# Kernel optimization log

Measured on AMD Instinct MI355X. Metric: run time of the kernel, lower is better.

Reference implementation:

```python
import jax, jax.numpy as jnp
import numpy as np

N_NODES = 50000
N_EDGES = 3200000
N_GRAPHS = 50
IN_FEATS, HIDDEN, OUT_FEATS = 5, 64, 2


def setup_inputs() -> dict:
    key = jax.random.key(0)
    ks = jax.random.split(key, 10)
    x = jax.random.normal(ks[0], (N_NODES, IN_FEATS), dtype=jnp.float32)
    edge_index = jax.random.randint(ks[1], (2, N_EDGES), 0, N_NODES, dtype=jnp.int64)
    edge_attr = jax.random.uniform(ks[2], (N_EDGES, 1), dtype=jnp.float32)
    batch = jnp.sort(jax.random.randint(ks[3], (N_NODES,), 0, N_GRAPHS, dtype=jnp.int64))
    s1 = 1.0 / np.sqrt(IN_FEATS)
    s2 = 1.0 / np.sqrt(HIDDEN)
    W1 = jax.random.uniform(ks[4], (IN_FEATS, HIDDEN), jnp.float32, -s1, s1)
    b1 = jnp.zeros((HIDDEN,), jnp.float32)
    W2 = jax.random.uniform(ks[5], (HIDDEN, HIDDEN), jnp.float32, -s2, s2)
    b2 = jnp.zeros((HIDDEN,), jnp.float32)
    Wo = jax.random.uniform(ks[6], (HIDDEN, OUT_FEATS), jnp.float32, -s2, s2)
    bo = jax.random.uniform(ks[7], (OUT_FEATS,), jnp.float32, -s2, s2)
    return {"x": x, "edge_index": edge_index, "edge_attr": edge_attr, "batch": batch,
            "W1": W1, "b1": b1, "W2": W2, "b2": b2, "Wo": Wo, "bo": bo}


def _gcn_conv(x, src, dst, ew, W, b):
    # symmetric normalization: D^{-1/2} (A + I) D^{-1/2}, weighted degrees
    deg = jax.ops.segment_sum(ew, dst, num_segments=N_NODES)
    dinv = jnp.where(deg > 0, jax.lax.rsqrt(jnp.where(deg > 0, deg, 1.0)), 0.0)
    norm = dinv[src] * ew * dinv[dst]  # [E+N]
    h = x @ W                           # transform before propagate (PyG order)
    msg = h[src] * norm[:, None]        # gather + scale per edge
    out = jax.ops.segment_sum(msg, dst, num_segments=N_NODES)
    return out + b


def reference(x, edge_index, edge_attr, batch, W1, b1, W2, b2, Wo, bo):
    ew = edge_attr.squeeze(-1)
    loop = jnp.arange(N_NODES, dtype=edge_index.dtype)  # add self-loops (GCNConv default)
    src = jnp.concatenate([edge_index[0], loop])
    dst = jnp.concatenate([edge_index[1], loop])
    ew = jnp.concatenate([ew, jnp.ones((N_NODES,), ew.dtype)])
    h = jax.nn.relu(_gcn_conv(x, src, dst, ew, W1, b1))
    h = jax.nn.relu(_gcn_conv(h, src, dst, ew, W2, b2))
    # global mean pool over graphs
    sums = jax.ops.segment_sum(h, batch, num_segments=N_GRAPHS)
    cnt = jax.ops.segment_sum(jnp.ones((N_NODES,), h.dtype), batch, num_segments=N_GRAPHS)
    pooled = sums / jnp.maximum(cnt, 1.0)[:, None]
    return pooled @ Wo + bo  # [N_GRAPHS, OUT_FEATS]
```

## Files before the change

kernel.cpp:

```cpp
#include <hip/hip_runtime.h>
#include <hip/hip_fp16.h>

#define N_NODES 50000
#define N_EDGES 3200000
#define N_GRAPHS 50
#define IN_F 5
#define HID 64
#define OUT_F 2

#define BKT_SHIFT 5
#define BKT_W 32
#define NBKT 1563
#define NB1 250
#define EPB 12800
#define CAP 2560
#define TILE_SHIFT 12
#define NTILE 16
#define NBIN (BKT_W * NTILE)
#define NWAVE 8192

__global__ void k_bhist(const int* dst, unsigned short* cw) {
    __shared__ int hist[NBKT];
    int t = threadIdx.x, blk = blockIdx.x;
    for (int b = t; b < NBKT; b += 256) hist[b] = 0;
    __syncthreads();
    int base = blk * EPB;
    for (int i = 0; i < EPB / 256; ++i) {
        int d = dst[base + i * 256 + t];
        atomicAdd(&hist[d >> BKT_SHIFT], 1);
    }
    __syncthreads();
    for (int b = t; b < NBKT; b += 256)
        cw[b * NB1 + blk] = (unsigned short)hist[b];
}

__global__ void k_bscanA(unsigned short* cw, int* total) {
    __shared__ int s[256];
    int t = threadIdx.x, b = blockIdx.x;
    int v = (t < NB1) ? (int)cw[b * NB1 + t] : 0;
    s[t] = v;
    __syncthreads();
    for (int off = 1; off < 256; off <<= 1) {
        int a = (t >= off) ? s[t - off] : 0;
        __syncthreads();
        s[t] += a;
        __syncthreads();
    }
    if (t < NB1) cw[b * NB1 + t] = (unsigned short)(s[t] - v);
    if (t == 255) total[b] = s[255];
}

__global__ void k_bscanB(const int* total, int* rpB) {
    __shared__ int s[256];
    int t = threadIdx.x;
    int v[7], sum = 0;
#pragma unroll
    for (int j = 0; j < 7; ++j) {
        int idx = t * 7 + j;
        v[j] = (idx < NBKT) ? total[idx] : 0;
        sum += v[j];
    }
    s[t] = sum;
    __syncthreads();
    for (int off = 1; off < 256; off <<= 1) {
        int a = (t >= off) ? s[t - off] : 0;
        __syncthreads();
        s[t] += a;
        __syncthreads();
    }
    int run = s[t] - sum;
#pragma unroll
    for (int j = 0; j < 7; ++j) {
        int idx = t * 7 + j;
        if (idx < NBKT) rpB[idx] = run;
        run += v[j];
    }
    if (t == 0) rpB[NBKT] = N_EDGES;
}

__global__ void k_bucket(const int* src, const int* dst, const float* ew,
                         const unsigned short* cw, const int* rpB, int2* bkt) {
    __shared__ int base[NBKT];
    __shared__ int off[NBKT];
    int t = threadIdx.x, blk = blockIdx.x;
    for (int b = t; b < NBKT; b += 256) {
        base[b] = (int)cw[b * NB1 + blk] + rpB[b];
        off[b] = 0;
    }
    __syncthreads();
    int ebase = blk * EPB;
    for (int i = 0; i < EPB / 256; ++i) {
        int idx = ebase + i * 256 + t;
        int d = dst[idx];
        int b = d >> BKT_SHIFT;
        int sl = base[b] + atomicAdd(&off[b], 1);
        bkt[sl] = make_int2(src[idx] | ((d & (BKT_W - 1)) << 16), __float_as_int(ew[idx]));
    }
}

__global__ void k_bsort(const int* rpB, int2* bkt, int* rp2, int* rp2e, float* dinv) {
    __shared__ int2 ebuf[CAP];
    __shared__ int hist[NBIN];
    __shared__ int binoff[NBIN];
    __shared__ int s[256];
    __shared__ float wd[BKT_W];
    int t = threadIdx.x, b = blockIdx.x;
    int e0 = rpB[b], cnt = rpB[b + 1] - e0;
    for (int i = t; i < NBIN; i += 256) hist[i] = 0;
    if (t < BKT_W) wd[t] = 0.f;
    __syncthreads();
    for (int k = t; k < cnt; k += 256) {
        int2 e = bkt[e0 + k];
        ebuf[k] = e;
        int dl = (e.x >> 16) & (BKT_W - 1);
        int bin = (dl << 4) | ((e.x & 0xFFFF) >> TILE_SHIFT);
        atomicAdd(&hist[bin], 1);
        atomicAdd(&wd[dl], __int_as_float(e.y));
    }
    __syncthreads();
    int h0 = hist[2 * t], h1 = hist[2 * t + 1];
    int pv = h0 + h1;
    s[t] = pv;
    __syncthreads();
    for (int off = 1; off < 256; off <<= 1) {
        int a = (t >= off) ? s[t - off] : 0;
        __syncthreads();
        s[t] += a;
        __syncthreads();
    }
    int pe = s[t] - pv;
    binoff[2 * t] = pe;
    binoff[2 * t + 1] = pe + h0;
    __syncthreads();
    if (t < BKT_W) {
        int node = (b << BKT_SHIFT) + t;
        if (node < N_NODES) {
            int startl = binoff[t << 4];
            int endl = (t == BKT_W - 1) ? cnt : binoff[(t + 1) << 4];
            rp2[node]  = 2 * e0 + startl;
            rp2e[node] = 2 * e0 + endl;
            dinv[node] = rsqrtf(1.0f + wd[t]);
        }
    }
    __syncthreads();
    for (int k = t; k < cnt; k += 256) {
        int2 e = ebuf[k];
        int dl = (e.x >> 16) & (BKT_W - 1);
        int bin = (dl << 4) | ((e.x & 0xFFFF) >> TILE_SHIFT);
        int pos = atomicAdd(&binoff[bin], 1);
        unsigned short wh = __half_as_ushort(__float2half(__int_as_float(e.y)));
        ((int*)bkt)[2 * e0 + pos] = (e.x & 0xFFFF) | ((int)wh << 16);
    }
}

__global__ void k_xprep(const float* x, const float* dinv, __half* xp) {
    int i = blockIdx.x * 256 + threadIdx.x;
    if (i < N_NODES) {
        float di = dinv[i];
        const float* xi = &x[i * IN_F];
        __half* o = &xp[i * 8];
#pragma unroll
        for (int f = 0; f < IN_F; ++f) o[f] = __float2half(xi[f] * di);
        o[5] = o[6] = o[7] = __float2half(0.f);
    }
}

__global__ void k_p(const int* rp2, const int* rp2e, const int* pk,
                    const __half* xp, const float* dinv, float* p) {
    int node = blockIdx.x * 4 + (threadIdx.x >> 6);
    int lane = threadIdx.x & 63;
    if (node >= N_NODES) return;
    int b = rp2[node], en = rp2e[node];
    float a0 = 0.f, a1 = 0.f, a2 = 0.f, a3 = 0.f, a4 = 0.f;
    for (int k = b + lane; k < en; k += 64) {
        int e = pk[k];
        float w = __half2float(__ushort_as_half((unsigned short)((unsigned)e >> 16)));
        const __half* xs = &xp[(e & 0xFFFF) * 8];
        int4 xv = *reinterpret_cast<const int4*>(xs);
        __half2 p01 = *(__half2*)&xv.x;
        __half2 p23 = *(__half2*)&xv.y;
        __half2 p45 = *(__half2*)&xv.z;
        a0 += w * __half2float(p01.x); a1 += w * __half2float(p01.y);
        a2 += w * __half2float(p23.x); a3 += w * __half2float(p23.y);
        a4 += w * __half2float(p45.x);
    }
    for (int off = 32; off; off >>= 1) {
        a0 += __shfl_down(a0, off); a1 += __shfl_down(a1, off); a2 += __shfl_down(a2, off);
        a3 += __shfl_down(a3, off); a4 += __shfl_down(a4, off);
    }
    if (lane == 0) {
        float di = dinv[node];
        const __half* xn = &xp[node * 8];
        float* pp = &p[node * IN_F];
        pp[0] = di * (a0 + __half2float(xn[0]));
        pp[1] = di * (a1 + __half2float(xn[1]));
        pp[2] = di * (a2 + __half2float(xn[2]));
        pp[3] = di * (a3 + __half2float(xn[3]));
        pp[4] = di * (a4 + __half2float(xn[4]));
    }
}

__global__ void k_h1g(const float* p, const float* W1, const float* b1,
                      const float* W2, const float* dinv, __half* g) {
    __shared__ float W1s[IN_F * HID];
    __shared__ float W2s[HID * HID];
    __shared__ float b1s[HID];
    int t = threadIdx.x;
    for (int k = t; k < IN_F * HID; k += 256) W1s[k] = W1[k];
    for (int k = t; k < HID * HID; k += 256) W2s[k] = W2[k];
    if (t < HID) b1s[t] = b1[t];
    __syncthreads();
    int lane = t & 63;
    int wid = blockIdx.x * 4 + (t >> 6);
    int nw = gridDim.x * 4;
    for (int node = wid; node < N_NODES; node += nw) {
        const float* pp = &p[node * IN_F];
        float pv0 = pp[0], pv1 = pp[1], pv2 = pp[2], pv3 = pp[3], pv4 = pp[4];
        float h = b1s[lane] + pv0 * W1s[lane] + pv1 * W1s[64 + lane] + pv2 * W1s[128 + lane]
                + pv3 * W1s[192 + lane] + pv4 * W1s[256 + lane];
        h = fmaxf(h, 0.f);
        float acc = 0.f;
#pragma unroll
        for (int f = 0; f < HID; ++f) {
            float hf = __int_as_float(__builtin_amdgcn_readlane(__float_as_int(h), f));
            acc += hf * W2s[f * HID + lane];
        }
        g[node * HID + lane] = __float2half(acc * dinv[node]);
    }
}

__global__ __launch_bounds__(256, 8) void k_h2g(const int* rp2, const int* rp2e,
                      const int* pk, const float* dinv, const __half* g,
                      const float* b2, const int* batch, float* pool) {
    int t = threadIdx.x, lane = t & 63;
    int wid = blockIdx.x * 4 + (t >> 6);
    int n0 = (int)(((long long)wid * N_NODES) / NWAVE);
    int n1 = (int)(((long long)(wid + 1) * N_NODES) / NWAVE);
    if (n0 >= n1) return;
    float bj = b2[lane];
    float accp = 0.f;
    int cur = batch[n0];
    for (int node = n0; node < n1; ++node) {
        int k0 = rp2[node], e1 = rp2e[node];
        float acc = __half2float(g[node * HID + lane]);
        for (; k0 < e1; k0 += 64) {
            int kk = k0 + lane;
            int ev = (kk < e1) ? pk[kk] : 0;
            int m = e1 - k0; if (m > 64) m = 64;
            int ng = (m + 15) >> 4;
            for (int q = 0; q < ng; ++q) {
                float vv[16], ww[16];
#pragma unroll
                for (int j = 0; j < 16; ++j) {
                    int u = __builtin_amdgcn_readlane(ev, q * 16 + j);
                    ww[j] = __half2float(__ushort_as_half((unsigned short)((unsigned)u >> 16)));
                    vv[j] = __half2float(g[(u & 0xFFFF) * HID + lane]);
                }
#pragma unroll
                for (int j = 0; j < 16; ++j) acc += vv[j] * ww[j];
            }
        }
        float h2 = fmaxf(dinv[node] * acc + bj, 0.f);
        int bb = batch[node];
        if (bb != cur) {
            atomicAdd(&pool[cur * HID + lane], accp);
            cur = bb;
            accp = 0.f;
        }
        accp += h2;
    }
    atomicAdd(&pool[cur * HID + lane], accp);
}

__device__ int lowb(const int* a, int n, int v) {
    int lo = 0, hi = n;
    while (lo < hi) { int m = (lo + hi) >> 1; if (a[m] < v) lo = m + 1; else hi = m; }
    return lo;
}

__global__ void k_out(const float* pool, const int* batch, const float* Wo,
                      const float* bo, float* out) {
    int t = blockIdx.x * blockDim.x + threadIdx.x;
    if (t < N_GRAPHS * OUT_F) {
        int gi = t / OUT_F, k = t % OUT_F;
        int c = lowb(batch, N_NODES, gi + 1) - lowb(batch, N_NODES, gi);
        float cf = fmaxf((float)c, 1.0f);
        float acc = bo[k];
        for (int f = 0; f < HID; ++f)
            acc += (pool[gi * HID + f] / cf) * Wo[f * OUT_F + k];
        out[t] = acc;
    }
}

extern "C" void kernel_launch(void* const* d_in, const int* in_sizes, int n_in,
                              void* d_out, int out_size, void* d_ws, size_t ws_size,
                              hipStream_t stream) {
    const float* x   = (const float*)d_in[0];
    const int*   ei  = (const int*)d_in[1];
    const float* ea  = (const float*)d_in[2];
    const int*   bat = (const int*)d_in[3];
    const float* W1  = (const float*)d_in[4];
    const float* b1  = (const float*)d_in[5];
    const float* W2  = (const float*)d_in[6];
    const float* b2  = (const float*)d_in[7];
    const float* Wo  = (const float*)d_in[8];
    const float* bo  = (const float*)d_in[9];
    float* out = (float*)d_out;

    const int* src = ei;
    const int* dst = ei + N_EDGES;

    float* ws = (float*)d_ws;
    int*   rpB   = (int*)ws;
    int*   rp2   = (int*)(ws + 1568);
    int*   rp2e  = (int*)(ws + 51584);
    float* dinv  = ws + 101600;
    float* pool  = ws + 151616;
    int*   total = (int*)(ws + 151616);
    unsigned short* cw = (unsigned short*)(ws + 154816);
    float* p     = ws + 154816;
    int2*  bkt   = (int2*)(ws + 404816);
    __half* g    = (__half*)(ws + 6804816);
    __half* xp   = (__half*)(ws + 8404816);

    k_bhist <<<NB1, 256, 0, stream>>>(dst, cw);
    k_bscanA<<<NBKT, 256, 0, stream>>>(cw, total);
    k_bscanB<<<1, 256, 0, stream>>>(total, rpB);
    hipMemsetAsync(pool, 0, N_GRAPHS * HID * sizeof(float), stream);
    k_bucket<<<NB1, 256, 0, stream>>>(src, dst, ea, cw, rpB, bkt);
    k_bsort <<<NBKT, 256, 0, stream>>>(rpB, bkt, rp2, rp2e, dinv);
    k_xprep <<<(N_NODES + 255) / 256, 256, 0, stream>>>(x, dinv, xp);
    k_p     <<<(N_NODES + 3) / 4, 256, 0, stream>>>(rp2, rp2e, (const int*)bkt, xp, dinv, p);
    k_h1g   <<<1024, 256, 0, stream>>>(p, W1, b1, W2, dinv, g);
    k_h2g   <<<NWAVE / 4, 256, 0, stream>>>(rp2, rp2e, (const int*)bkt, dinv, g, b2, bat, pool);
    k_out   <<<1, 128, 0, stream>>>(pool, bat, Wo, bo, out);
}
```

Before: 336.4 us.

## Replace stable bucket scatter with atomic-cursor fill and quantize hidden features to int8

The bucketing pipeline changes from a per-block histogram with a two-level scan and stable scatter to global atomic bucket counts, a single scan, and a per-edge atomic-cursor fill. This removes the cw matrix and one scan kernel. Order within a bucket becomes nondeterministic, but the later per-bucket sort handles it. The layer-2 features g are also stored as int8 with a per-node scale instead of fp16, halving gather traffic in k_h2g at the cost of quantization error and an extra per-edge scale load.

```diff
diff --git a/kernel.cpp b/kernel.cpp
--- a/kernel.cpp
+++ b/kernel.cpp
@@ -11,34 +11,38 @@
 #define BKT_SHIFT 5
 #define BKT_W 32
 #define NBKT 1563
-#define NB1 250
-#define EPB 12800
 #define CAP 2560
 #define TILE_SHIFT 12
-#define NTILE 16
-#define NBIN (BKT_W * NTILE)
+#define NBIN (BKT_W * 16)
 #define NWAVE 8192
-
-__global__ void k_bhist(const int* dst, unsigned short* cw) {
+#define EPC 6250
+
+__global__ void k_cnt(const int* dst, int* total) {
     __shared__ int hist[NBKT];
     int t = threadIdx.x, blk = blockIdx.x;
     for (int b = t; b < NBKT; b += 256) hist[b] = 0;
     __syncthreads();
-    int base = blk * EPB;
-    for (int i = 0; i < EPB / 256; ++i) {
-        int d = dst[base + i * 256 + t];
-        atomicAdd(&hist[d >> BKT_SHIFT], 1);
-    }
-    __syncthreads();
-    for (int b = t; b < NBKT; b += 256)
-        cw[b * NB1 + blk] = (unsigned short)hist[b];
-}
-
-__global__ void k_bscanA(unsigned short* cw, int* total) {
+    int base = blk * EPC;
+    for (int k = t; k < EPC; k += 256)
+        atomicAdd(&hist[dst[base + k] >> BKT_SHIFT], 1);
+    __syncthreads();
+    for (int b = t; b < NBKT; b += 256) {
+        int h = hist[b];
+        if (h) atomicAdd(&total[b], h);
+    }
+}
+
+__global__ void k_scan(const int* total, int* rpB, int* cursor) {
     __shared__ int s[256];
-    int t = threadIdx.x, b = blockIdx.x;
-    int v = (t < NB1) ? (int)cw[b * NB1 + t] : 0;
-    s[t] = v;
+    int t = threadIdx.x;
+    int v[7], sum = 0;
+#pragma unroll
+    for (int j = 0; j < 7; ++j) {
+        int idx = t * 7 + j;
+        v[j] = (idx < NBKT) ? total[idx] : 0;
+        sum += v[j];
+    }
+    s[t] = sum;
     __syncthreads();
     for (int off = 1; off < 256; off <<= 1) {
         int a = (t >= off) ? s[t - off] : 0;
@@ -46,56 +50,23 @@
         s[t] += a;
         __syncthreads();
     }
-    if (t < NB1) cw[b * NB1 + t] = (unsigned short)(s[t] - v);
-    if (t == 255) total[b] = s[255];
-}
-
-__global__ void k_bscanB(const int* total, int* rpB) {
-    __shared__ int s[256];
-    int t = threadIdx.x;
-    int v[7], sum = 0;
+    int run = s[t] - sum;
 #pragma unroll
     for (int j = 0; j < 7; ++j) {
         int idx = t * 7 + j;
-        v[j] = (idx < NBKT) ? total[idx] : 0;
-        sum += v[j];
-    }
-    s[t] = sum;
-    __syncthreads();
-    for (int off = 1; off < 256; off <<= 1) {
-        int a = (t >= off) ? s[t - off] : 0;
-        __syncthreads();
-        s[t] += a;
-        __syncthreads();
-    }
-    int run = s[t] - sum;
-#pragma unroll
-    for (int j = 0; j < 7; ++j) {
-        int idx = t * 7 + j;
-        if (idx < NBKT) rpB[idx] = run;
+        if (idx < NBKT) { rpB[idx] = run; cursor[idx] = run; }
         run += v[j];
     }
     if (t == 0) rpB[NBKT] = N_EDGES;
 }
 
-__global__ void k_bucket(const int* src, const int* dst, const float* ew,
-                         const unsigned short* cw, const int* rpB, int2* bkt) {
-    __shared__ int base[NBKT];
-    __shared__ int off[NBKT];
-    int t = threadIdx.x, blk = blockIdx.x;
-    for (int b = t; b < NBKT; b += 256) {
-        base[b] = (int)cw[b * NB1 + blk] + rpB[b];
-        off[b] = 0;
-    }
-    __syncthreads();
-    int ebase = blk * EPB;
-    for (int i = 0; i < EPB / 256; ++i) {
-        int idx = ebase + i * 256 + t;
-        int d = dst[idx];
-        int b = d >> BKT_SHIFT;
-        int sl = base[b] + atomicAdd(&off[b], 1);
-        bkt[sl] = make_int2(src[idx] | ((d & (BKT_W - 1)) << 16), __float_as_int(ew[idx]));
-    }
+__global__ void k_fill(const int* src, const int* dst, const float* ew,
+                       int* cursor, int2* bkt) {
+    int e = blockIdx.x * 256 + threadIdx.x;
+    int d = dst[e];
+    int b = d >> BKT_SHIFT;
+    int slot = atomicAdd(&cursor[b], 1);
+    bkt[slot] = make_int2(src[e] | ((d & (BKT_W - 1)) << 16), __float_as_int(ew[e]));
 }
 
 __global__ void k_bsort(const int* rpB, int2* bkt, int* rp2, int* rp2e, float* dinv) {
@@ -201,7 +172,8 @@
 }
 
 __global__ void k_h1g(const float* p, const float* W1, const float* b1,
-                      const float* W2, const float* dinv, __half* g) {
+                      const float* W2, const float* dinv,
+                      signed char* g8, float* rs) {
     __shared__ float W1s[IN_F * HID];
     __shared__ float W2s[HID * HID];
     __shared__ float b1s[HID];
@@ -225,13 +197,18 @@
             float hf = __int_as_float(__builtin_amdgcn_readlane(__float_as_int(h), f));
             acc += hf * W2s[f * HID + lane];
         }
-        g[node * HID + lane] = __float2half(acc * dinv[node]);
+        float gv = acc * dinv[node];
+        float am = fabsf(gv);
+        for (int off = 32; off; off >>= 1) am = fmaxf(am, __shfl_xor(am, off));
+        float inv = (am > 0.f) ? 127.0f / am : 0.f;
+        g8[node * HID + lane] = (signed char)__float2int_rn(gv * inv);
+        if (lane == 0) rs[node] = (am > 0.f) ? am * (1.0f / 127.0f) : 0.f;
     }
 }
 
 __global__ __launch_bounds__(256, 8) void k_h2g(const int* rp2, const int* rp2e,
-                      const int* pk, const float* dinv, const __half* g,
-                      const float* b2, const int* batch, float* pool) {
+                      const int* pk, const float* dinv, const signed char* g8,
+                      const float* rs, const float* b2, const int* batch, float* pool) {
     int t = threadIdx.x, lane = t & 63;
     int wid = blockIdx.x * 4 + (t >> 6);
     int n0 = (int)(((long long)wid * N_NODES) / NWAVE);
@@ -242,7 +219,7 @@
     int cur = batch[n0];
     for (int node = n0; node < n1; ++node) {
         int k0 = rp2[node], e1 = rp2e[node];
-        float acc = __half2float(g[node * HID + lane]);
+        float acc = (float)g8[node * HID + lane] * rs[node];
         for (; k0 < e1; k0 += 64) {
             int kk = k0 + lane;
             int ev = (kk < e1) ? pk[kk] : 0;
@@ -253,8 +230,10 @@
 #pragma unroll
                 for (int j = 0; j < 16; ++j) {
                     int u = __builtin_amdgcn_readlane(ev, q * 16 + j);
-                    ww[j] = __half2float(__ushort_as_half((unsigned short)((unsigned)u >> 16)));
-                    vv[j] = __half2float(g[(u & 0xFFFF) * HID + lane]);
+                    int sx = u & 0xFFFF;
+                    float w = __half2float(__ushort_as_half((unsigned short)((unsigned)u >> 16)));
+                    ww[j] = w * rs[sx];
+                    vv[j] = (float)g8[sx * HID + lane];
                 }
 #pragma unroll
                 for (int j = 0; j < 16; ++j) acc += vv[j] * ww[j];
@@ -311,27 +290,29 @@
     const int* dst = ei + N_EDGES;
 
     float* ws = (float*)d_ws;
-    int*   rpB   = (int*)ws;
-    int*   rp2   = (int*)(ws + 1568);
-    int*   rp2e  = (int*)(ws + 51584);
-    float* dinv  = ws + 101600;
-    float* pool  = ws + 151616;
-    int*   total = (int*)(ws + 151616);
-    unsigned short* cw = (unsigned short*)(ws + 154816);
-    float* p     = ws + 154816;
-    int2*  bkt   = (int2*)(ws + 404816);
-    __half* g    = (__half*)(ws + 6804816);
-    __half* xp   = (__half*)(ws + 8404816);
-
-    k_bhist <<<NB1, 256, 0, stream>>>(dst, cw);
-    k_bscanA<<<NBKT, 256, 0, stream>>>(cw, total);
-    k_bscanB<<<1, 256, 0, stream>>>(total, rpB);
+    int*   rpB    = (int*)ws;
+    int*   cursor = (int*)(ws + 1568);
+    int*   rp2    = (int*)(ws + 3136);
+    int*   rp2e   = (int*)(ws + 53152);
+    float* dinv   = ws + 103168;
+    float* rs     = ws + 153184;
+    float* pool   = ws + 203200;
+    int*   total  = (int*)(ws + 206400);
+    float* p      = ws + 207968;
+    int2*  bkt    = (int2*)(ws + 457968);
+    signed char* g8 = (signed char*)(ws + 6857968);
+    __half* xp    = (__half*)(ws + 7657968);
+
+    hipMemsetAsync(total, 0, NBKT * sizeof(int), stream);
     hipMemsetAsync(pool, 0, N_GRAPHS * HID * sizeof(float), stream);
-    k_bucket<<<NB1, 256, 0, stream>>>(src, dst, ea, cw, rpB, bkt);
-    k_bsort <<<NBKT, 256, 0, stream>>>(rpB, bkt, rp2, rp2e, dinv);
-    k_xprep <<<(N_NODES + 255) / 256, 256, 0, stream>>>(x, dinv, xp);
-    k_p     <<<(N_NODES + 3) / 4, 256, 0, stream>>>(rp2, rp2e, (const int*)bkt, xp, dinv, p);
-    k_h1g   <<<1024, 256, 0, stream>>>(p, W1, b1, W2, dinv, g);
-    k_h2g   <<<NWAVE / 4, 256, 0, stream>>>(rp2, rp2e, (const int*)bkt, dinv, g, b2, bat, pool);
-    k_out   <<<1, 128, 0, stream>>>(pool, bat, Wo, bo, out);
-}
+
+    k_cnt  <<<512, 256, 0, stream>>>(dst, total);
+    k_scan <<<1, 256, 0, stream>>>(total, rpB, cursor);
+    k_fill <<<N_EDGES / 256, 256, 0, stream>>>(src, dst, ea, cursor, bkt);
+    k_bsort<<<NBKT, 256, 0, stream>>>(rpB, bkt, rp2, rp2e, dinv);
+    k_xprep<<<(N_NODES + 255) / 256, 256, 0, stream>>>(x, dinv, xp);
+    k_p    <<<(N_NODES + 3) / 4, 256, 0, stream>>>(rp2, rp2e, (const int*)bkt, xp, dinv, p);
+    k_h1g  <<<1024, 256, 0, stream>>>(p, W1, b1, W2, dinv, g8, rs);
+    k_h2g  <<<NWAVE / 4, 256, 0, stream>>>(rp2, rp2e, (const int*)bkt, dinv, g8, rs, b2, bat, pool);
+    k_out  <<<1, 128, 0, stream>>>(pool, bat, Wo, bo, out);
+}
```

After: 755.9 us. 125% more time.
